# Performance work log

Measured on AMD Instinct MI355X. Metric: run time of the kernel, lower is better.

## Reference

```python
import jax, jax.numpy as jnp
import numpy as np

B, D, K = 32768, 256, 1024


def setup_inputs() -> dict:
    key = jax.random.key(0)
    k1, k2 = jax.random.split(key)
    embedding = jax.random.normal(k1, (B, D), dtype=jnp.float32)
    codebook = jax.random.normal(k2, (K, D), dtype=jnp.float32)
    return {"embedding": embedding, "codebook": codebook}


def reference(embedding, codebook):
    # code_norms: (K,) squared L2 norm of each code
    code_norms = jnp.sum(codebook ** 2, axis=1)            # (K,)
    dots = embedding @ codebook.T                           # (B, K)
    alpha = dots / code_norms[None, :]                      # (B, K)
    # error for projecting e onto line of code c:
    #   ||e - alpha c||^2 = ||e||^2 - dots^2 / ||c||^2
    # (identical math to materializing (B,K,D) diff, without the blowup)
    e_norms = jnp.sum(embedding ** 2, axis=1, keepdims=True)  # (B, 1)
    errors = e_norms - dots ** 2 / code_norms[None, :]        # (B, K)
    indices = jnp.argmin(errors, axis=1)                      # (B,)
    # gather chosen projection: alpha[b, idx[b]] * codebook[idx[b]]
    alpha_sel = jnp.take_along_axis(alpha, indices[:, None], axis=1)  # (B, 1)
    z_out = alpha_sel * codebook[indices]                     # (B, D)
    return (z_out, indices)
```

## Files before the change

kernel.cpp:

```cpp
#include <hip/hip_runtime.h>
#include <cstdint>

#define B_ROWS 32768
#define DIM    256
#define KCODES 1024
#define NSPLIT 2

typedef _Float16 f16x8 __attribute__((ext_vector_type(8)));
typedef float    f32x4 __attribute__((ext_vector_type(4)));


__global__ __launch_bounds__(64) void vq_prep(const float* __restrict__ cb,
                                              _Float16* __restrict__ hi,
                                              _Float16* __restrict__ lo,
                                              float* __restrict__ inv_norm) {
  const int k = blockIdx.x;
  const int lane = threadIdx.x;
  float4 c = reinterpret_cast<const float4*>(cb)[k * 64 + lane];
  float nrm = c.x * c.x + c.y * c.y + c.z * c.z + c.w * c.w;
#pragma unroll
  for (int off = 32; off; off >>= 1) nrm += __shfl_xor(nrm, off);
  if (lane == 0) inv_norm[k] = 1.0f / nrm;

  float f[4] = {c.x, c.y, c.z, c.w};
  _Float16 h[4], l[4];
#pragma unroll
  for (int i = 0; i < 4; ++i) {
    h[i] = (_Float16)f[i];
    l[i] = (_Float16)((f[i] - (float)h[i]) * 2048.0f);
  }
  const int phys = (lane >> 1) ^ (k & 15);
  const int byteoff = k * 512 + phys * 16 + (lane & 1) * 8;
  *reinterpret_cast<uint2*>((char*)hi + byteoff) = *reinterpret_cast<uint2*>(h);
  *reinterpret_cast<uint2*>((char*)lo + byteoff) = *reinterpret_cast<uint2*>(l);
}

__device__ __forceinline__ void gld16(const void* g, void* l) {
  __builtin_amdgcn_global_load_lds(
      (const __attribute__((address_space(1))) uint32_t*)g,
      (__attribute__((address_space(3))) uint32_t*)l, 16, 0, 0);
}

#define MFMA16(a, b, acc) __builtin_amdgcn_mfma_f32_16x16x32_f16((a), (b), (acc), 0, 0, 0)

__global__ __launch_bounds__(256, 2) void vq_main(const float* __restrict__ emb,
                                                  const _Float16* __restrict__ cbh,
                                                  const _Float16* __restrict__ cbl,
                                                  const float* __restrict__ inv_g,
                                                  float2* __restrict__ cand) {
  __shared__ uint4 Btile[4][1024];
  __shared__ float inv_s[KCODES];

  const int flat = threadIdx.x;
  const int wave = flat >> 6;
  const int lane = flat & 63;
  const int quad = lane >> 4;
  const int lr   = lane & 15;

  const int b = blockIdx.x;
  const int rowblk = ((b >> 4) << 3) | (b & 7);
  const int split  = (b >> 3) & 1;
  const int t0 = split * 32;
  const int tend = t0 + 32;

  reinterpret_cast<float4*>(inv_s)[flat] = reinterpret_cast<const float4*>(inv_g)[flat];

  f16x8 Ah[2][8], Al[2][8];
  const int row0 = rowblk * 128 + wave * 32;
#pragma unroll
  for (int s = 0; s < 2; ++s) {
    const float* rp = emb + (size_t)(row0 + s * 16 + lr) * DIM;
#pragma unroll
    for (int c = 0; c < 8; ++c) {
      const float* p = rp + c * 32 + quad * 8;
      float4 f0 = *reinterpret_cast<const float4*>(p);
      float4 f1 = *reinterpret_cast<const float4*>(p + 4);
      float f[8] = {f0.x, f0.y, f0.z, f0.w, f1.x, f1.y, f1.z, f1.w};
      f16x8 h, l;
#pragma unroll
      for (int j = 0; j < 8; ++j) {
        _Float16 hv = (_Float16)f[j];
        h[j] = hv;
        l[j] = (_Float16)((f[j] - (float)hv) * 2048.0f);
      }
      Ah[s][c] = h;
      Al[s][c] = l;
    }
  }

  __syncthreads();

  auto stage = [&](int t) {
    const char* srcH = (const char*)cbh + t * 8192;
    const char* srcL = (const char*)cbl + t * 8192;
    char* dst = (char*)&Btile[t & 3][0];
    const int off = flat * 16;
    gld16(srcH + off,        dst + off);
    gld16(srcH + 4096 + off, dst + 4096 + off);
    gld16(srcL + off,        dst + 8192 + off);
    gld16(srcL + 4096 + off, dst + 12288 + off);
  };
  stage(t0);
  stage(t0 + 1);
  stage(t0 + 2);

  float bg[2][4], bd[2][4];
  int   bk[2][4];
#pragma unroll
  for (int s = 0; s < 2; ++s)
#pragma unroll
    for (int r = 0; r < 4; ++r) { bg[s][r] = -1.0f; bd[s][r] = 0.0f; bk[s][r] = t0 * 16; }

  for (int t = t0; t < tend; ++t) {
    const int rem = tend - t;
    if (rem >= 3)      asm volatile("s_waitcnt vmcnt(8)" ::: "memory");
    else if (rem == 2) asm volatile("s_waitcnt vmcnt(4)" ::: "memory");
    else               asm volatile("s_waitcnt vmcnt(0)" ::: "memory");
    __builtin_amdgcn_sched_barrier(0);
    __builtin_amdgcn_s_barrier();
    __builtin_amdgcn_sched_barrier(0);

    const char* buf = (const char*)&Btile[t & 3][0];

    f32x4 aA0  = {0, 0, 0, 0}, aA1  = {0, 0, 0, 0};
    f32x4 aBa0 = {0, 0, 0, 0}, aBa1 = {0, 0, 0, 0};
    f32x4 aBb0 = {0, 0, 0, 0}, aBb1 = {0, 0, 0, 0};

    {
      f16x8 bh[4], bl[4];
#pragma unroll
      for (int c = 0; c < 4; ++c) {
        const int g = (((c * 4 + quad) ^ lr) * 16) + lr * 512;
        bh[c] = *reinterpret_cast<const f16x8*>(buf + g);
        bl[c] = *reinterpret_cast<const f16x8*>(buf + 8192 + g);
      }
      if (rem > 3) stage(t + 3);
      __builtin_amdgcn_sched_barrier(0);
      __builtin_amdgcn_s_barrier();
      asm volatile("s_waitcnt lgkmcnt(0)" ::: "memory");
      __builtin_amdgcn_sched_barrier(0);
      __builtin_amdgcn_s_setprio(1);
#pragma unroll
      for (int c = 0; c < 4; ++c) {
        aA0  = MFMA16(Ah[0][c], bh[c], aA0);
        aA1  = MFMA16(Ah[1][c], bh[c], aA1);
        aBa0 = MFMA16(Al[0][c], bh[c], aBa0);
        aBa1 = MFMA16(Al[1][c], bh[c], aBa1);
        aBb0 = MFMA16(Ah[0][c], bl[c], aBb0);
        aBb1 = MFMA16(Ah[1][c], bl[c], aBb1);
      }
      __builtin_amdgcn_s_setprio(0);
      __builtin_amdgcn_sched_barrier(0);
    }

    {
      f16x8 bh[4], bl[4];
#pragma unroll
      for (int c = 0; c < 4; ++c) {
        const int g = ((((c + 4) * 4 + quad) ^ lr) * 16) + lr * 512;
        bh[c] = *reinterpret_cast<const f16x8*>(buf + g);
        bl[c] = *reinterpret_cast<const f16x8*>(buf + 8192 + g);
      }
      __builtin_amdgcn_sched_barrier(0);
      __builtin_amdgcn_s_barrier();
      asm volatile("s_waitcnt lgkmcnt(0)" ::: "memory");
      __builtin_amdgcn_sched_barrier(0);
      __builtin_amdgcn_s_setprio(1);
#pragma unroll
      for (int c = 0; c < 4; ++c) {
        aA0  = MFMA16(Ah[0][c + 4], bh[c], aA0);
        aA1  = MFMA16(Ah[1][c + 4], bh[c], aA1);
        aBa0 = MFMA16(Al[0][c + 4], bh[c], aBa0);
        aBa1 = MFMA16(Al[1][c + 4], bh[c], aBa1);
        aBb0 = MFMA16(Ah[0][c + 4], bl[c], aBb0);
        aBb1 = MFMA16(Ah[1][c + 4], bl[c], aBb1);
      }
      __builtin_amdgcn_s_setprio(0);
      __builtin_amdgcn_sched_barrier(0);
    }

    const int n = t * 16 + lr;
    const float inl = inv_s[n];
#pragma unroll
    for (int r = 0; r < 4; ++r) {
      float d0 = aA0[r] + (aBa0[r] + aBb0[r]) * 4.8828125e-4f;
      float g0 = d0 * d0 * inl;
      if (g0 > bg[0][r]) { bg[0][r] = g0; bd[0][r] = d0; bk[0][r] = n; }
      float d1 = aA1[r] + (aBa1[r] + aBb1[r]) * 4.8828125e-4f;
      float g1 = d1 * d1 * inl;
      if (g1 > bg[1][r]) { bg[1][r] = g1; bd[1][r] = d1; bk[1][r] = n; }
    }
  }

#pragma unroll
  for (int s = 0; s < 2; ++s) {
#pragma unroll
    for (int r = 0; r < 4; ++r) {
      float g = bg[s][r]; int k = bk[s][r]; float d = bd[s][r];
#pragma unroll
      for (int m = 1; m < 16; m <<= 1) {
        float g2 = __shfl_xor(g, m);
        int   k2 = __shfl_xor(k, m);
        float d2 = __shfl_xor(d, m);
        if (g2 > g || (g2 == g && k2 < k)) { g = g2; k = k2; d = d2; }
      }
      if (lr == 0) {
        const int row = row0 + s * 16 + quad * 4 + r;
        cand[(size_t)split * B_ROWS + row] = make_float2(d, __int_as_float(k));
      }
    }
  }
}

__global__ __launch_bounds__(256) void vq_reduce(const float2* __restrict__ cand,
                                                 const float* __restrict__ inv_g,
                                                 const float* __restrict__ cb,
                                                 float* __restrict__ out) {
  const int wave = threadIdx.x >> 6;
  const int lane = threadIdx.x & 63;
  const int row = blockIdx.x * 4 + wave;

  float best_g = -1.0f, best_d = 0.0f;
  int best_k = 0;
#pragma unroll
  for (int s = 0; s < NSPLIT; ++s) {
    float2 c = cand[(size_t)s * B_ROWS + row];
    int k = __float_as_int(c.y);
    float g = c.x * c.x * inv_g[k];
    if (g > best_g || (g == best_g && k < best_k)) {
      best_g = g; best_d = c.x; best_k = k;
    }
  }
  const float alpha = best_d * inv_g[best_k];
  float4 c4 = reinterpret_cast<const float4*>(cb)[best_k * 64 + lane];
  float4 z = {alpha * c4.x, alpha * c4.y, alpha * c4.z, alpha * c4.w};
  reinterpret_cast<float4*>(out)[(size_t)row * 64 + lane] = z;
  if (lane == 0) out[(size_t)B_ROWS * DIM + row] = (float)best_k;
}

extern "C" void kernel_launch(void* const* d_in, const int* in_sizes, int n_in,
                              void* d_out, int out_size, void* d_ws, size_t ws_size,
                              hipStream_t stream) {
  const float* emb = (const float*)d_in[0];
  const float* cb  = (const float*)d_in[1];
  _Float16* cbh = (_Float16*)d_ws;
  _Float16* cbl = (_Float16*)((char*)d_ws + (512 << 10));
  float*    inv = (float*)((char*)d_ws + (1 << 20));
  float2*   cand = (float2*)((char*)d_ws + (1 << 20) + 4096);

  vq_prep<<<KCODES, 64, 0, stream>>>(cb, cbh, cbl, inv);
  vq_main<<<(B_ROWS / 128) * NSPLIT, 256, 0, stream>>>(emb, cbh, cbl, inv, cand);
  vq_reduce<<<B_ROWS / 4, 256, 0, stream>>>(cand, inv, cb, (float*)d_out);
}
```

Before: 140.0 us.

## Fuse split reduction and gather into main kernel via last-block ticket

Removes the separate reduce kernel launch. Each of the two split blocks for a row block bumps an atomic ticket in workspace, and the second block to arrive merges both candidate lists, gathers codebook rows and writes the outputs. The prep kernel resets the tickets on every call. This saves a launch and a pass over the candidates, but the final gather and store work is serialized onto half the blocks at the tail and depends on acquire/release ordering through the atomic.

```diff
diff --git a/kernel.cpp b/kernel.cpp
--- a/kernel.cpp
+++ b/kernel.cpp
@@ -13,9 +13,11 @@
 __global__ __launch_bounds__(64) void vq_prep(const float* __restrict__ cb,
                                               _Float16* __restrict__ hi,
                                               _Float16* __restrict__ lo,
-                                              float* __restrict__ inv_norm) {
+                                              float* __restrict__ inv_norm,
+                                              unsigned* __restrict__ ticket) {
   const int k = blockIdx.x;
   const int lane = threadIdx.x;
+  if (k < 256 && lane == 0) ticket[k] = 0u;
   float4 c = reinterpret_cast<const float4*>(cb)[k * 64 + lane];
   float nrm = c.x * c.x + c.y * c.y + c.z * c.z + c.w * c.w;
 #pragma unroll
@@ -47,9 +49,13 @@
                                                   const _Float16* __restrict__ cbh,
                                                   const _Float16* __restrict__ cbl,
                                                   const float* __restrict__ inv_g,
-                                                  float2* __restrict__ cand) {
+                                                  float2* __restrict__ cand,
+                                                  const float* __restrict__ cb32,
+                                                  float* __restrict__ out,
+                                                  unsigned* __restrict__ ticket) {
   __shared__ uint4 Btile[4][1024];
   __shared__ float inv_s[KCODES];
+  __shared__ int winner;
 
   const int flat = threadIdx.x;
   const int wave = flat >> 6;
@@ -210,32 +216,36 @@
       }
     }
   }
-}
-
-__global__ __launch_bounds__(256) void vq_reduce(const float2* __restrict__ cand,
-                                                 const float* __restrict__ inv_g,
-                                                 const float* __restrict__ cb,
-                                                 float* __restrict__ out) {
-  const int wave = threadIdx.x >> 6;
-  const int lane = threadIdx.x & 63;
-  const int row = blockIdx.x * 4 + wave;
-
-  float best_g = -1.0f, best_d = 0.0f;
-  int best_k = 0;
-#pragma unroll
-  for (int s = 0; s < NSPLIT; ++s) {
-    float2 c = cand[(size_t)s * B_ROWS + row];
-    int k = __float_as_int(c.y);
-    float g = c.x * c.x * inv_g[k];
-    if (g > best_g || (g == best_g && k < best_k)) {
-      best_g = g; best_d = c.x; best_k = k;
-    }
-  }
-  const float alpha = best_d * inv_g[best_k];
-  float4 c4 = reinterpret_cast<const float4*>(cb)[best_k * 64 + lane];
-  float4 z = {alpha * c4.x, alpha * c4.y, alpha * c4.z, alpha * c4.w};
-  reinterpret_cast<float4*>(out)[(size_t)row * 64 + lane] = z;
-  if (lane == 0) out[(size_t)B_ROWS * DIM + row] = (float)best_k;
+
+  __syncthreads();
+  if (flat == 0) {
+    unsigned old = __hip_atomic_fetch_add(&ticket[rowblk], 1u,
+                                          __ATOMIC_ACQ_REL, __HIP_MEMORY_SCOPE_AGENT);
+    winner = (old == 1u);
+  }
+  __syncthreads();
+  if (!winner) return;
+
+  const float2* __restrict__ c0p = cand;
+  const float2* __restrict__ c1p = cand + B_ROWS;
+#pragma unroll 4
+  for (int i = 0; i < 32; ++i) {
+    const int row = rowblk * 128 + i * 4 + wave;
+    float2 ca = c0p[row];
+    float2 cbv = c1p[row];
+    int k0 = __float_as_int(ca.y);
+    int k1 = __float_as_int(cbv.y);
+    float ga = ca.x * ca.x * inv_s[k0];
+    float gb = cbv.x * cbv.x * inv_s[k1];
+    float d_; int k_;
+    if (ga > gb || (ga == gb && k0 < k1)) { d_ = ca.x; k_ = k0; }
+    else                                  { d_ = cbv.x; k_ = k1; }
+    const float alpha = d_ * inv_s[k_];
+    float4 c4 = reinterpret_cast<const float4*>(cb32)[k_ * 64 + lane];
+    f32x4 z = {alpha * c4.x, alpha * c4.y, alpha * c4.z, alpha * c4.w};
+    __builtin_nontemporal_store(z, reinterpret_cast<f32x4*>(out) + (size_t)row * 64 + lane);
+    if (lane == 0) out[(size_t)B_ROWS * DIM + row] = (float)k_;
+  }
 }
 
 extern "C" void kernel_launch(void* const* d_in, const int* in_sizes, int n_in,
@@ -247,8 +257,9 @@
   _Float16* cbl = (_Float16*)((char*)d_ws + (512 << 10));
   float*    inv = (float*)((char*)d_ws + (1 << 20));
   float2*   cand = (float2*)((char*)d_ws + (1 << 20) + 4096);
-
-  vq_prep<<<KCODES, 64, 0, stream>>>(cb, cbh, cbl, inv);
-  vq_main<<<(B_ROWS / 128) * NSPLIT, 256, 0, stream>>>(emb, cbh, cbl, inv, cand);
-  vq_reduce<<<B_ROWS / 4, 256, 0, stream>>>(cand, inv, cb, (float*)d_out);
-}
+  unsigned* ticket = (unsigned*)((char*)d_ws + (1 << 20) + 4096 + (512 << 10));
+
+  vq_prep<<<KCODES, 64, 0, stream>>>(cb, cbh, cbl, inv, ticket);
+  vq_main<<<(B_ROWS / 128) * NSPLIT, 256, 0, stream>>>(emb, cbh, cbl, inv, cand,
+                                                       cb, (float*)d_out, ticket);
+}
```

Result: slower. 151.5 us (+8.2%).

## Load low-half codebook directly into registers, halve LDS tile, batch reduce rows

Applied to the files above, without the earlier changes.

The low-order fp16 codebook correction is now read straight from global memory into registers, software-prefetched one half-tile ahead, instead of being staged through LDS. The prep kernel writes it unswizzled so each lane can load it contiguously. This halves LDS traffic and the shared-memory footprint but puts more vector memory loads and vmcnt bookkeeping on each wave. The reduce kernel also handles four rows per wave with nontemporal output stores, cutting the block count.

```diff
diff --git a/kernel.cpp b/kernel.cpp
--- a/kernel.cpp
+++ b/kernel.cpp
@@ -29,10 +29,11 @@
     h[i] = (_Float16)f[i];
     l[i] = (_Float16)((f[i] - (float)h[i]) * 2048.0f);
   }
-  const int phys = (lane >> 1) ^ (k & 15);
-  const int byteoff = k * 512 + phys * 16 + (lane & 1) * 8;
-  *reinterpret_cast<uint2*>((char*)hi + byteoff) = *reinterpret_cast<uint2*>(h);
-  *reinterpret_cast<uint2*>((char*)lo + byteoff) = *reinterpret_cast<uint2*>(l);
+  const int physH = (lane >> 1) ^ (k & 15);
+  const int offH = k * 512 + physH * 16 + (lane & 1) * 8;
+  *reinterpret_cast<uint2*>((char*)hi + offH) = *reinterpret_cast<uint2*>(h);
+  const int offL = k * 512 + lane * 8;
+  *reinterpret_cast<uint2*>((char*)lo + offL) = *reinterpret_cast<uint2*>(l);
 }
 
 __device__ __forceinline__ void gld16(const void* g, void* l) {
@@ -48,7 +49,7 @@
                                                   const _Float16* __restrict__ cbl,
                                                   const float* __restrict__ inv_g,
                                                   float2* __restrict__ cand) {
-  __shared__ uint4 Btile[4][1024];
+  __shared__ uint4 Btile[4][512];
   __shared__ float inv_s[KCODES];
 
   const int flat = threadIdx.x;
@@ -92,17 +93,26 @@
 
   auto stage = [&](int t) {
     const char* srcH = (const char*)cbh + t * 8192;
-    const char* srcL = (const char*)cbl + t * 8192;
     char* dst = (char*)&Btile[t & 3][0];
     const int off = flat * 16;
     gld16(srcH + off,        dst + off);
     gld16(srcH + 4096 + off, dst + 4096 + off);
-    gld16(srcL + off,        dst + 8192 + off);
-    gld16(srcL + 4096 + off, dst + 12288 + off);
   };
+  auto blload4 = [&](f16x8 (&dst)[4], int t, int c0) {
+    const char* p = (const char*)cbl + (size_t)t * 8192
+                  + (size_t)(lr * 512 + quad * 16 + c0 * 64);
+#pragma unroll
+    for (int j = 0; j < 4; ++j)
+      dst[j] = *reinterpret_cast<const f16x8*>(p + j * 64);
+  };
+
+  f16x8 cur0[4], cur1[4];
   stage(t0);
   stage(t0 + 1);
   stage(t0 + 2);
+  blload4(cur0, t0, 0);
+  asm volatile("s_waitcnt vmcnt(8)" ::: "memory");
+  __builtin_amdgcn_s_barrier();
 
   float bg[2][4], bd[2][4];
   int   bk[2][4];
@@ -113,13 +123,6 @@
 
   for (int t = t0; t < tend; ++t) {
     const int rem = tend - t;
-    if (rem >= 3)      asm volatile("s_waitcnt vmcnt(8)" ::: "memory");
-    else if (rem == 2) asm volatile("s_waitcnt vmcnt(4)" ::: "memory");
-    else               asm volatile("s_waitcnt vmcnt(0)" ::: "memory");
-    __builtin_amdgcn_sched_barrier(0);
-    __builtin_amdgcn_s_barrier();
-    __builtin_amdgcn_sched_barrier(0);
-
     const char* buf = (const char*)&Btile[t & 3][0];
 
     f32x4 aA0  = {0, 0, 0, 0}, aA1  = {0, 0, 0, 0};
@@ -127,17 +130,20 @@
     f32x4 aBb0 = {0, 0, 0, 0}, aBb1 = {0, 0, 0, 0};
 
     {
-      f16x8 bh[4], bl[4];
+      f16x8 bh[4];
 #pragma unroll
       for (int c = 0; c < 4; ++c) {
         const int g = (((c * 4 + quad) ^ lr) * 16) + lr * 512;
         bh[c] = *reinterpret_cast<const f16x8*>(buf + g);
-        bl[c] = *reinterpret_cast<const f16x8*>(buf + 8192 + g);
-      }
+      }
+      blload4(cur1, t, 4);
+      __builtin_amdgcn_sched_barrier(0);
+      __builtin_amdgcn_s_barrier();
       if (rem > 3) stage(t + 3);
-      __builtin_amdgcn_sched_barrier(0);
-      __builtin_amdgcn_s_barrier();
       asm volatile("s_waitcnt lgkmcnt(0)" ::: "memory");
+      __builtin_amdgcn_sched_barrier(0);
+      if (rem > 3) asm volatile("s_waitcnt vmcnt(6)" ::: "memory");
+      else         asm volatile("s_waitcnt vmcnt(4)" ::: "memory");
       __builtin_amdgcn_sched_barrier(0);
       __builtin_amdgcn_s_setprio(1);
 #pragma unroll
@@ -146,24 +152,28 @@
         aA1  = MFMA16(Ah[1][c], bh[c], aA1);
         aBa0 = MFMA16(Al[0][c], bh[c], aBa0);
         aBa1 = MFMA16(Al[1][c], bh[c], aBa1);
-        aBb0 = MFMA16(Ah[0][c], bl[c], aBb0);
-        aBb1 = MFMA16(Ah[1][c], bl[c], aBb1);
+        aBb0 = MFMA16(Ah[0][c], cur0[c], aBb0);
+        aBb1 = MFMA16(Ah[1][c], cur0[c], aBb1);
       }
       __builtin_amdgcn_s_setprio(0);
       __builtin_amdgcn_sched_barrier(0);
     }
 
     {
-      f16x8 bh[4], bl[4];
+      f16x8 bh[4];
 #pragma unroll
       for (int c = 0; c < 4; ++c) {
         const int g = ((((c + 4) * 4 + quad) ^ lr) * 16) + lr * 512;
         bh[c] = *reinterpret_cast<const f16x8*>(buf + g);
-        bl[c] = *reinterpret_cast<const f16x8*>(buf + 8192 + g);
-      }
+      }
+      if (rem >= 2) blload4(cur0, t + 1, 0);
       __builtin_amdgcn_sched_barrier(0);
       __builtin_amdgcn_s_barrier();
       asm volatile("s_waitcnt lgkmcnt(0)" ::: "memory");
+      __builtin_amdgcn_sched_barrier(0);
+      if (rem > 3)       asm volatile("s_waitcnt vmcnt(6)" ::: "memory");
+      else if (rem >= 2) asm volatile("s_waitcnt vmcnt(4)" ::: "memory");
+      else               asm volatile("s_waitcnt vmcnt(0)" ::: "memory");
       __builtin_amdgcn_sched_barrier(0);
       __builtin_amdgcn_s_setprio(1);
 #pragma unroll
@@ -172,8 +182,8 @@
         aA1  = MFMA16(Ah[1][c + 4], bh[c], aA1);
         aBa0 = MFMA16(Al[0][c + 4], bh[c], aBa0);
         aBa1 = MFMA16(Al[1][c + 4], bh[c], aBa1);
-        aBb0 = MFMA16(Ah[0][c + 4], bl[c], aBb0);
-        aBb1 = MFMA16(Ah[1][c + 4], bl[c], aBb1);
+        aBb0 = MFMA16(Ah[0][c + 4], cur1[c], aBb0);
+        aBb1 = MFMA16(Ah[1][c + 4], cur1[c], aBb1);
       }
       __builtin_amdgcn_s_setprio(0);
       __builtin_amdgcn_sched_barrier(0);
@@ -218,24 +228,26 @@
                                                  float* __restrict__ out) {
   const int wave = threadIdx.x >> 6;
   const int lane = threadIdx.x & 63;
-  const int row = blockIdx.x * 4 + wave;
-
-  float best_g = -1.0f, best_d = 0.0f;
-  int best_k = 0;
-#pragma unroll
-  for (int s = 0; s < NSPLIT; ++s) {
-    float2 c = cand[(size_t)s * B_ROWS + row];
-    int k = __float_as_int(c.y);
-    float g = c.x * c.x * inv_g[k];
-    if (g > best_g || (g == best_g && k < best_k)) {
-      best_g = g; best_d = c.x; best_k = k;
-    }
-  }
-  const float alpha = best_d * inv_g[best_k];
-  float4 c4 = reinterpret_cast<const float4*>(cb)[best_k * 64 + lane];
-  float4 z = {alpha * c4.x, alpha * c4.y, alpha * c4.z, alpha * c4.w};
-  reinterpret_cast<float4*>(out)[(size_t)row * 64 + lane] = z;
-  if (lane == 0) out[(size_t)B_ROWS * DIM + row] = (float)best_k;
+  const int base = blockIdx.x * 16;
+
+#pragma unroll
+  for (int i = 0; i < 4; ++i) {
+    const int row = base + i * 4 + wave;
+    float2 ca = cand[row];
+    float2 cbv = cand[(size_t)B_ROWS + row];
+    int k0 = __float_as_int(ca.y);
+    int k1 = __float_as_int(cbv.y);
+    float ga = ca.x * ca.x * inv_g[k0];
+    float gb = cbv.x * cbv.x * inv_g[k1];
+    float d_; int k_;
+    if (ga > gb || (ga == gb && k0 < k1)) { d_ = ca.x; k_ = k0; }
+    else                                  { d_ = cbv.x; k_ = k1; }
+    const float alpha = d_ * inv_g[k_];
+    float4 c4 = reinterpret_cast<const float4*>(cb)[k_ * 64 + lane];
+    f32x4 z = {alpha * c4.x, alpha * c4.y, alpha * c4.z, alpha * c4.w};
+    __builtin_nontemporal_store(z, reinterpret_cast<f32x4*>(out) + (size_t)row * 64 + lane);
+    if (lane == 0) out[(size_t)B_ROWS * DIM + row] = (float)k_;
+  }
 }
 
 extern "C" void kernel_launch(void* const* d_in, const int* in_sizes, int n_in,
@@ -250,5 +262,5 @@
 
   vq_prep<<<KCODES, 64, 0, stream>>>(cb, cbh, cbl, inv);
   vq_main<<<(B_ROWS / 128) * NSPLIT, 256, 0, stream>>>(emb, cbh, cbl, inv, cand);
-  vq_reduce<<<B_ROWS / 4, 256, 0, stream>>>(cand, inv, cb, (float*)d_out);
-}
+  vq_reduce<<<B_ROWS / 16, 256, 0, stream>>>(cand, inv, cb, (float*)d_out);
+}
```

Measured after the change: 162.3 us. 1.16x slower.
